# Kernel tuning notes

Measured on AMD Instinct MI355X. Metric: run time of the kernel, lower is better.

## Reference

```python
import jax, jax.numpy as jnp
import numpy as np

B, K, D, O = 8192, 256, 128, 8

def setup_inputs() -> dict:
    key = jax.random.key(0)
    k1, k2, k3 = jax.random.split(key, 3)
    x = jax.random.normal(k1, (B, D), dtype=jnp.float32)
    centers = jax.random.normal(k2, (K, D), dtype=jnp.float32)  # init.normal_(centers, 0, 1)
    shapes = jnp.ones((K,), dtype=jnp.float32)                  # init.constant_(shapes, 1)
    W = jax.random.normal(k3, (O, K), dtype=jnp.float32) * (1.0 / np.sqrt(K))
    b = jnp.zeros((O,), dtype=jnp.float32)
    return {"x": x, "centers": centers, "shapes": shapes, "W": W, "b": b}

def reference(x, centers, shapes, W, b):
    x2 = jnp.sum(x * x, axis=-1, keepdims=True)            # (B, 1)
    c2 = jnp.sum(centers * centers, axis=-1)               # (K,)
    xc = x @ centers.T                                     # (B, K)
    sqdist = jnp.maximum(x2 - 2.0 * xc + c2, 0.0)          # (B, K) = dist^2
    # phi = exp(-(dist * shape)^2) = exp(-sqdist * shape^2)
    phi = jnp.exp(-sqdist * (shapes * shapes))             # (B, K)
    # normalization=False in this config
    return phi @ W.T + b                                   # (B, O)
```

## Files before the change

kernel.cpp:

```cpp
#include <hip/hip_runtime.h>
#include <hip/hip_bf16.h>


typedef __attribute__((ext_vector_type(8))) short bf16x8;
typedef __attribute__((ext_vector_type(4))) float f32x4;

static __device__ __forceinline__ ushort f2bf(float f) {
    __hip_bfloat16 h = __float2bfloat16(f);
    ushort u;
    __builtin_memcpy(&u, &h, 2);
    return u;
}
static __device__ __forceinline__ bf16x8 pack8(float4 a, float4 b) {
    bf16x8 v;
    v[0] = (short)f2bf(a.x); v[1] = (short)f2bf(a.y);
    v[2] = (short)f2bf(a.z); v[3] = (short)f2bf(a.w);
    v[4] = (short)f2bf(b.x); v[5] = (short)f2bf(b.y);
    v[6] = (short)f2bf(b.z); v[7] = (short)f2bf(b.w);
    return v;
}
static __device__ __forceinline__ float dot4(float4 a) {
    return a.x * a.x + a.y * a.y + a.z * a.z + a.w * a.w;
}

#define NT 512

__global__ __launch_bounds__(NT, 2)
void rbf_r8(const float* __restrict__ x, const float* __restrict__ centers,
            const float* __restrict__ shapes, const float* __restrict__ W,
            const float* __restrict__ bias, float* __restrict__ out)
{
    __shared__ ushort Al[8 * 64 * 8];
    __shared__ ushort WTl[16 * 256];
    __shared__ ushort Pl[8][32 * 64];
    __shared__ float  red[8][32][8];
    __shared__ float  x2p[32][17];
    __shared__ float  x2s[32];

    const int t    = threadIdx.x;
    const int lane = t & 63;
    const int w    = t >> 6;
    const int g    = lane >> 4;
    const int l15  = lane & 15;
    const int row0 = blockIdx.x * 32;
    const int n0   = w * 32;

    const int xr = t >> 4, xc8 = t & 15;
    const float* xp = x + (size_t)(row0 + xr) * 128 + xc8 * 8;
    float4 xa = *(const float4*)(xp);
    float4 xb = *(const float4*)(xp + 4);

    float4 bv[2][8];
    #pragma unroll
    for (int nt = 0; nt < 2; ++nt) {
        const float* cp = centers + (size_t)(n0 + nt * 16 + l15) * 128 + g * 8;
        #pragma unroll
        for (int d = 0; d < 4; ++d) {
            bv[nt][2 * d]     = *(const float4*)(cp + d * 32);
            bv[nt][2 * d + 1] = *(const float4*)(cp + d * 32 + 4);
        }
    }

    const int wo = t >> 5, wk = (t & 31) * 8;
    float4 wv0, wv1;
    if (wo < 8) {
        wv0 = *(const float4*)(W + wo * 256 + wk);
        wv1 = *(const float4*)(W + wo * 256 + wk + 4);
    }

    float s2n[2];
    #pragma unroll
    for (int nt = 0; nt < 2; ++nt) {
        float s = shapes[n0 + nt * 16 + l15];
        s2n[nt] = s * s;
    }

    x2p[xr][xc8] = dot4(xa) + dot4(xb);
    {
        int mt = xr >> 4, d = xc8 >> 2, gg = xc8 & 3;
        int ll = gg * 16 + (xr & 15);
        *(bf16x8*)(Al + ((mt * 4 + d) * 64 + ll) * 8) = pack8(xa, xb);
    }

    {
        bf16x8 v;
        if (wo < 8) v = pack8(wv0, wv1);
        else        v = bf16x8{0, 0, 0, 0, 0, 0, 0, 0};
        *(bf16x8*)((char*)WTl + ((wo * 512 + wk * 2) ^ ((wo & 7) << 4))) = v;
    }

    bf16x8 bf[2][4];
    float  c2v[2];
    #pragma unroll
    for (int nt = 0; nt < 2; ++nt) {
        float c2 = 0.f;
        #pragma unroll
        for (int d = 0; d < 4; ++d)
            c2 += dot4(bv[nt][2 * d]) + dot4(bv[nt][2 * d + 1]);
        c2 += __shfl_xor(c2, 16);
        c2 += __shfl_xor(c2, 32);
        c2v[nt] = c2;
        #pragma unroll
        for (int d = 0; d < 4; ++d)
            bf[nt][d] = pack8(bv[nt][2 * d], bv[nt][2 * d + 1]);
    }

    __syncthreads();

    if (t < 32) {
        float s = 0.f;
        #pragma unroll
        for (int i = 0; i < 16; ++i) s += x2p[t][i];
        x2s[t] = s;
    }

    bf16x8 af[2][4];
    #pragma unroll
    for (int mt = 0; mt < 2; ++mt)
        #pragma unroll
        for (int d = 0; d < 4; ++d)
            af[mt][d] = *(bf16x8*)(Al + ((mt * 4 + d) * 64 + lane) * 8);

    f32x4 acc[2][2];
    #pragma unroll
    for (int mt = 0; mt < 2; ++mt)
        #pragma unroll
        for (int nt = 0; nt < 2; ++nt) acc[mt][nt] = f32x4{0.f, 0.f, 0.f, 0.f};

    #pragma unroll
    for (int d = 0; d < 4; ++d) {
        acc[0][0] = __builtin_amdgcn_mfma_f32_16x16x32_bf16(af[0][d], bf[0][d], acc[0][0], 0, 0, 0);
        acc[1][0] = __builtin_amdgcn_mfma_f32_16x16x32_bf16(af[1][d], bf[0][d], acc[1][0], 0, 0, 0);
        acc[0][1] = __builtin_amdgcn_mfma_f32_16x16x32_bf16(af[0][d], bf[1][d], acc[0][1], 0, 0, 0);
        acc[1][1] = __builtin_amdgcn_mfma_f32_16x16x32_bf16(af[1][d], bf[1][d], acc[1][1], 0, 0, 0);
    }

    __syncthreads();

    float x2r[2][4];
    #pragma unroll
    for (int mt = 0; mt < 2; ++mt)
        #pragma unroll
        for (int r = 0; r < 4; ++r) x2r[mt][r] = x2s[mt * 16 + g * 4 + r];

    char* pw = (char*)&Pl[w][0];
    #pragma unroll
    for (int nt = 0; nt < 2; ++nt) {
        float ns2  = -s2n[nt];
        int   kcol = nt * 16 + l15;
        #pragma unroll
        for (int mt = 0; mt < 2; ++mt)
            #pragma unroll
            for (int r = 0; r < 4; ++r) {
                int   row = mt * 16 + g * 4 + r;
                float arg = fmaf(-2.f, acc[mt][nt][r], x2r[mt][r] + c2v[nt]);
                float phi = __expf(fmaxf(arg, 0.f) * ns2);
                *(ushort*)(pw + ((row * 128 + kcol * 2) ^ ((row & 7) << 4))) = f2bf(phi);
            }
    }

    bf16x8 wf = *(bf16x8*)((char*)WTl + ((l15 * 512 + (n0 + g * 8) * 2) ^ ((l15 & 7) << 4)));
    #pragma unroll
    for (int mt = 0; mt < 2; ++mt) {
        int prow = mt * 16 + l15;
        bf16x8 pa = *(bf16x8*)(pw + ((prow * 128 + g * 16) ^ ((prow & 7) << 4)));
        f32x4 dacc = __builtin_amdgcn_mfma_f32_16x16x32_bf16(pa, wf,
                     f32x4{0.f, 0.f, 0.f, 0.f}, 0, 0, 0);
        if (l15 < 8) {
            #pragma unroll
            for (int r = 0; r < 4; ++r) red[w][mt * 16 + g * 4 + r][l15] = dacc[r];
        }
    }
    __syncthreads();

    if (t < 256) {
        int row = t >> 3, o = t & 7;
        float s = bias[o];
        #pragma unroll
        for (int ww = 0; ww < 8; ++ww) s += red[ww][row][o];
        out[(size_t)(row0 + row) * 8 + o] = s;
    }
}

extern "C" void kernel_launch(void* const* d_in, const int* in_sizes, int n_in,
                              void* d_out, int out_size, void* d_ws, size_t ws_size,
                              hipStream_t stream) {
    const float* x       = (const float*)d_in[0];
    const float* centers = (const float*)d_in[1];
    const float* shapes  = (const float*)d_in[2];
    const float* W       = (const float*)d_in[3];
    const float* bias    = (const float*)d_in[4];
    float* out           = (float*)d_out;

    const int Brows = in_sizes[0] / 128;
    hipLaunchKernelGGL(rbf_r8, dim3(Brows / 32), dim3(NT), 0, stream,
                       x, centers, shapes, W, bias, out);
}
```

Measured before the change: 11.70 us.

## Stage centers cooperatively in swizzled LDS instead of per-wave strided register loads

All 512 threads load the full 256x128 centers matrix with coalesced 64-byte-per-thread reads, convert it to bf16, and store it in a 64 KB XOR-swizzled shared buffer. Partial center norms are reduced through shared memory, and shapes squared are staged in shared memory as well. Each wave then reads its B fragments from LDS inside the MFMA loop. This replaces the earlier per-lane strided global loads and shuffle reductions. LDS use per block grows from about 32 KB to roughly 107 KB, which may cut occupancy below the two blocks per CU the launch bounds assume.

```diff
diff --git a/kernel.cpp b/kernel.cpp
--- a/kernel.cpp
+++ b/kernel.cpp
@@ -26,16 +26,18 @@
 #define NT 512
 
 __global__ __launch_bounds__(NT, 2)
-void rbf_r8(const float* __restrict__ x, const float* __restrict__ centers,
+void rbf_r9(const float* __restrict__ x, const float* __restrict__ centers,
             const float* __restrict__ shapes, const float* __restrict__ W,
             const float* __restrict__ bias, float* __restrict__ out)
 {
+    __shared__ ushort Bl[256 * 128];
     __shared__ ushort Al[8 * 64 * 8];
     __shared__ ushort WTl[16 * 256];
     __shared__ ushort Pl[8][32 * 64];
     __shared__ float  red[8][32][8];
+    __shared__ float  c2p[256][8];
     __shared__ float  x2p[32][17];
-    __shared__ float  x2s[32];
+    __shared__ float  c2f[256], s2f[256], x2s[32];
 
     const int t    = threadIdx.x;
     const int lane = t & 63;
@@ -46,72 +48,60 @@
     const int n0   = w * 32;
 
     const int xr = t >> 4, xc8 = t & 15;
-    const float* xp = x + (size_t)(row0 + xr) * 128 + xc8 * 8;
-    float4 xa = *(const float4*)(xp);
-    float4 xb = *(const float4*)(xp + 4);
-
-    float4 bv[2][8];
-    #pragma unroll
-    for (int nt = 0; nt < 2; ++nt) {
-        const float* cp = centers + (size_t)(n0 + nt * 16 + l15) * 128 + g * 8;
-        #pragma unroll
-        for (int d = 0; d < 4; ++d) {
-            bv[nt][2 * d]     = *(const float4*)(cp + d * 32);
-            bv[nt][2 * d + 1] = *(const float4*)(cp + d * 32 + 4);
-        }
+    {
+        const float* xp = x + (size_t)(row0 + xr) * 128 + xc8 * 8;
+        float4 xa = *(const float4*)(xp);
+        float4 xb = *(const float4*)(xp + 4);
+        x2p[xr][xc8] = dot4(xa) + dot4(xb);
+        int d = xc8 >> 2, gg = xc8 & 3;
+        int ll = gg * 16 + (xr & 15);
+        *(bf16x8*)(Al + (((xr >> 4) * 4 + d) * 64 + ll) * 8) = pack8(xa, xb);
     }
 
-    const int wo = t >> 5, wk = (t & 31) * 8;
-    float4 wv0, wv1;
-    if (wo < 8) {
-        wv0 = *(const float4*)(W + wo * 256 + wk);
-        wv1 = *(const float4*)(W + wo * 256 + wk + 4);
-    }
-
-    float s2n[2];
     #pragma unroll
-    for (int nt = 0; nt < 2; ++nt) {
-        float s = shapes[n0 + nt * 16 + l15];
-        s2n[nt] = s * s;
-    }
-
-    x2p[xr][xc8] = dot4(xa) + dot4(xb);
-    {
-        int mt = xr >> 4, d = xc8 >> 2, gg = xc8 & 3;
-        int ll = gg * 16 + (xr & 15);
-        *(bf16x8*)(Al + ((mt * 4 + d) * 64 + ll) * 8) = pack8(xa, xb);
+    for (int i = 0; i < 4; ++i) {
+        int id = t + NT * i;
+        int c = id >> 3, sg = id & 7;
+        const float* cp = centers + (size_t)c * 128 + sg * 16;
+        float4 b0 = *(const float4*)(cp);
+        float4 b1 = *(const float4*)(cp + 4);
+        float4 b2 = *(const float4*)(cp + 8);
+        float4 b3 = *(const float4*)(cp + 12);
+        c2p[c][sg] = dot4(b0) + dot4(b1) + dot4(b2) + dot4(b3);
+        char* bb = (char*)Bl;
+        *(bf16x8*)(bb + ((c * 256 + sg * 32) ^ ((c & 7) << 4)))      = pack8(b0, b1);
+        *(bf16x8*)(bb + ((c * 256 + sg * 32 + 16) ^ ((c & 7) << 4))) = pack8(b2, b3);
     }
 
     {
-        bf16x8 v;
-        if (wo < 8) v = pack8(wv0, wv1);
-        else        v = bf16x8{0, 0, 0, 0, 0, 0, 0, 0};
+        const int wo = t >> 5, wk = (t & 31) * 8;
+        bf16x8 v = {0, 0, 0, 0, 0, 0, 0, 0};
+        if (wo < 8) {
+            float4 w0 = *(const float4*)(W + wo * 256 + wk);
+            float4 w1 = *(const float4*)(W + wo * 256 + wk + 4);
+            v = pack8(w0, w1);
+        }
         *(bf16x8*)((char*)WTl + ((wo * 512 + wk * 2) ^ ((wo & 7) << 4))) = v;
     }
 
-    bf16x8 bf[2][4];
-    float  c2v[2];
-    #pragma unroll
-    for (int nt = 0; nt < 2; ++nt) {
-        float c2 = 0.f;
-        #pragma unroll
-        for (int d = 0; d < 4; ++d)
-            c2 += dot4(bv[nt][2 * d]) + dot4(bv[nt][2 * d + 1]);
-        c2 += __shfl_xor(c2, 16);
-        c2 += __shfl_xor(c2, 32);
-        c2v[nt] = c2;
-        #pragma unroll
-        for (int d = 0; d < 4; ++d)
-            bf[nt][d] = pack8(bv[nt][2 * d], bv[nt][2 * d + 1]);
+    if (t < 256) {
+        float s = shapes[t];
+        s2f[t] = s * s;
     }
 
     __syncthreads();
 
-    if (t < 32) {
+    if (t < 256) {
         float s = 0.f;
         #pragma unroll
-        for (int i = 0; i < 16; ++i) s += x2p[t][i];
-        x2s[t] = s;
+        for (int j = 0; j < 8; ++j) s += c2p[t][j];
+        c2f[t] = s;
+    } else if (t < 288) {
+        int u = t - 256;
+        float s = 0.f;
+        #pragma unroll
+        for (int j = 0; j < 16; ++j) s += x2p[u][j];
+        x2s[u] = s;
     }
 
     bf16x8 af[2][4];
@@ -128,32 +118,36 @@
         for (int nt = 0; nt < 2; ++nt) acc[mt][nt] = f32x4{0.f, 0.f, 0.f, 0.f};
 
     #pragma unroll
-    for (int d = 0; d < 4; ++d) {
-        acc[0][0] = __builtin_amdgcn_mfma_f32_16x16x32_bf16(af[0][d], bf[0][d], acc[0][0], 0, 0, 0);
-        acc[1][0] = __builtin_amdgcn_mfma_f32_16x16x32_bf16(af[1][d], bf[0][d], acc[1][0], 0, 0, 0);
-        acc[0][1] = __builtin_amdgcn_mfma_f32_16x16x32_bf16(af[0][d], bf[1][d], acc[0][1], 0, 0, 0);
-        acc[1][1] = __builtin_amdgcn_mfma_f32_16x16x32_bf16(af[1][d], bf[1][d], acc[1][1], 0, 0, 0);
+    for (int nt = 0; nt < 2; ++nt) {
+        int n = n0 + nt * 16 + l15;
+        #pragma unroll
+        for (int d = 0; d < 4; ++d) {
+            bf16x8 bf = *(bf16x8*)((char*)Bl + ((n * 256 + (g * 8 + d * 32) * 2) ^ ((n & 7) << 4)));
+            acc[0][nt] = __builtin_amdgcn_mfma_f32_16x16x32_bf16(af[0][d], bf, acc[0][nt], 0, 0, 0);
+            acc[1][nt] = __builtin_amdgcn_mfma_f32_16x16x32_bf16(af[1][d], bf, acc[1][nt], 0, 0, 0);
+        }
     }
 
     __syncthreads();
 
-    float x2r[2][4];
+    float4 x2q[2];
     #pragma unroll
     for (int mt = 0; mt < 2; ++mt)
-        #pragma unroll
-        for (int r = 0; r < 4; ++r) x2r[mt][r] = x2s[mt * 16 + g * 4 + r];
+        x2q[mt] = *(const float4*)(x2s + mt * 16 + g * 4);
 
     char* pw = (char*)&Pl[w][0];
     #pragma unroll
     for (int nt = 0; nt < 2; ++nt) {
-        float ns2  = -s2n[nt];
+        int   k    = n0 + nt * 16 + l15;
+        float c2   = c2f[k];
+        float ns2  = -s2f[k];
         int   kcol = nt * 16 + l15;
         #pragma unroll
         for (int mt = 0; mt < 2; ++mt)
             #pragma unroll
             for (int r = 0; r < 4; ++r) {
                 int   row = mt * 16 + g * 4 + r;
-                float arg = fmaf(-2.f, acc[mt][nt][r], x2r[mt][r] + c2v[nt]);
+                float arg = fmaf(-2.f, acc[mt][nt][r], x2q[mt][r] + c2);
                 float phi = __expf(fmaxf(arg, 0.f) * ns2);
                 *(ushort*)(pw + ((row * 128 + kcol * 2) ^ ((row & 7) << 4))) = f2bf(phi);
             }
@@ -193,6 +187,6 @@
     float* out           = (float*)d_out;
 
     const int Brows = in_sizes[0] / 128;
-    hipLaunchKernelGGL(rbf_r8, dim3(Brows / 32), dim3(NT), 0, stream,
+    hipLaunchKernelGGL(rbf_r9, dim3(Brows / 32), dim3(NT), 0, stream,
                        x, centers, shapes, W, bias, out);
 }
```

Measured after the change: 10.24 us. 1.14x faster.
